# Performance work log

Measured on AMD Instinct MI355X. Metric: run time of the kernel, lower is better.

Reference implementation:

```python
import jax, jax.numpy as jnp
import numpy as np

N_ATOMS = 262144
BATCH = 4096
HIDDEN = 256
HEADS = 4
SCALE = (HIDDEN // HEADS) ** -0.5
LN_EPS = 1e-5
SM_EPS = 1e-16


def setup_inputs() -> dict:
    key = jax.random.key(0)
    ks = jax.random.split(key, 10)
    s = HIDDEN ** -0.5
    return {
        "drug_atoms": jax.random.normal(ks[0], (N_ATOMS, HIDDEN), jnp.float32),
        "protein_ctx": jax.random.normal(ks[1], (BATCH, HIDDEN), jnp.float32),
        "batch_index": jnp.sort(jax.random.randint(ks[2], (N_ATOMS,), 0, BATCH)),
        "Wq": jax.random.normal(ks[3], (HIDDEN, HIDDEN), jnp.float32) * s,
        "bq": jnp.zeros((HIDDEN,), jnp.float32),
        "Wk": jax.random.normal(ks[4], (HIDDEN, HIDDEN), jnp.float32) * s,
        "bk": jnp.zeros((HIDDEN,), jnp.float32),
        "Wv": jax.random.normal(ks[5], (HIDDEN, HIDDEN), jnp.float32) * s,
        "bv": jnp.zeros((HIDDEN,), jnp.float32),
        "ln_gamma": jnp.ones((HIDDEN,), jnp.float32),
        "ln_beta": jnp.zeros((HIDDEN,), jnp.float32),
    }


def _segment_softmax(logits, seg, num_segments):
    # logits: [N, 1]; segment-wise stable softmax (torch_geometric.utils.softmax)
    m = jax.ops.segment_max(logits, seg, num_segments=num_segments)  # [B, 1]
    e = jnp.exp(logits - m[seg])
    s = jax.ops.segment_sum(e, seg, num_segments=num_segments)  # [B, 1]
    return e / (s[seg] + SM_EPS)


def _layer_norm(x, gamma, beta):
    mu = jnp.mean(x, axis=-1, keepdims=True)
    var = jnp.mean(jnp.square(x - mu), axis=-1, keepdims=True)
    return (x - mu) * jax.lax.rsqrt(var + LN_EPS) * gamma + beta


def reference(drug_atoms, protein_ctx, batch_index, Wq, bq, Wk, bk, Wv, bv, ln_gamma, ln_beta):
    protein_expanded = protein_ctx[batch_index]  # [N, H] gather
    Q = protein_expanded @ Wq + bq
    K = drug_atoms @ Wk + bk
    V = drug_atoms @ Wv + bv
    dots = jnp.sum(Q * K, axis=-1, keepdims=True) * SCALE  # [N, 1]
    attn = _segment_softmax(dots, batch_index, BATCH)  # [N, 1]
    out = attn * V + drug_atoms  # weighted V + residual
    return _layer_norm(out, ln_gamma, ln_beta), attn
```

## Files before the change

### kernel.cpp

```cpp
#include <hip/hip_runtime.h>
#include <hip/hip_bf16.h>

#define N_ATOMS 262144
#define BATCH   4096
#define HID     256

typedef __attribute__((ext_vector_type(8))) short short8;
typedef __attribute__((ext_vector_type(4))) float f32x4;
typedef unsigned short u16;
typedef unsigned int   u32;

__device__ __forceinline__ float bf2f(u16 h){
    u32 x = ((u32)h) << 16;
    return __builtin_bit_cast(float, x);
}
__device__ __forceinline__ u16 f2bf(float f){
    u32 x = __builtin_bit_cast(u32, f);
    u32 r = (x + 0x7FFFu + ((x >> 16) & 1u)) >> 16;
    return (u16)r;
}
__device__ __forceinline__ int probe_isf32(const u32* p){
    return ((p[0] & 0xFFFFu) == 0u) ? 1 : 0;
}
__device__ __forceinline__ float cvt_any(const void* p, size_t i, int isf32){
    return isf32 ? ((const float*)p)[i] : bf2f(((const u16*)p)[i]);
}

__global__ void prep_kernel(const void* Wq, const void* Wk, const void* Wv,
                            const void* bq, const void* bk, const void* bv,
                            const void* gamma, const void* beta,
                            float* __restrict__ WqTF, float* __restrict__ WkF,
                            u16* __restrict__ WvT,
                            u32* __restrict__ menc, float* __restrict__ sbuf,
                            float* __restrict__ bqf, float* __restrict__ bkf,
                            float* __restrict__ bvf, float* __restrict__ gamf,
                            float* __restrict__ betf){
    const int isf32 = probe_isf32((const u32*)gamma);
    int blk = blockIdx.x, t = threadIdx.x;
    if (blk < 256){
        WqTF[blk*HID + t] = cvt_any(Wq, (size_t)t*HID + blk, isf32);
    } else if (blk < 512){
        size_t i = (size_t)(blk - 256)*256 + t;
        WkF[i] = cvt_any(Wk, i, isf32);
    } else if (blk < 768){
        int j = blk - 512;
        WvT[j*HID + t] = f2bf(cvt_any(Wv, (size_t)t*HID + j, isf32));
    } else if (blk < 784){
        int i = (blk - 768)*256 + t;
        menc[i] = 0u; sbuf[i] = 0.f;
    } else {
        bqf[t]  = cvt_any(bq, t, isf32);
        bkf[t]  = cvt_any(bk, t, isf32);
        bvf[t]  = cvt_any(bv, t, isf32);
        gamf[t] = cvt_any(gamma, t, isf32);
        betf[t] = cvt_any(beta, t, isf32);
    }
}

template<int AMODE, int BIAS>
__global__ void small_gemm(const void* Araw, const float* __restrict__ BtF,
                           const float* __restrict__ biasF,
                           float* __restrict__ outF, const u32* __restrict__ probe){
    __shared__ float As[8*HID];
    const int t  = threadIdx.x;
    const int rb = blockIdx.x * 8;
    const int isf32 = AMODE ? 1 : probe_isf32(probe);
    #pragma unroll
    for (int i = 0; i < 8; ++i)
        As[i*HID + t] = cvt_any(Araw, (size_t)(rb + i)*HID + t, isf32);
    __syncthreads();
    float acc[8] = {0.f,0.f,0.f,0.f,0.f,0.f,0.f,0.f};
    for (int j = 0; j < HID; j += 4){
        float4 w = *(const float4*)(BtF + (size_t)t*HID + j);
        #pragma unroll
        for (int r = 0; r < 8; ++r){
            float4 a = *(const float4*)(As + r*HID + j);
            acc[r] += a.x*w.x + a.y*w.y + a.z*w.z + a.w*w.w;
        }
    }
    float b = BIAS ? biasF[t] : 0.f;
    #pragma unroll
    for (int r = 0; r < 8; ++r)
        outF[(size_t)(rb + r)*HID + t] = acc[r] + b;
}

__global__ void ck_kernel(const float* __restrict__ Qf, const float* __restrict__ bkf,
                          float* __restrict__ cvec){
    int row  = blockIdx.x*4 + (threadIdx.x >> 6);
    int lane = threadIdx.x & 63;
    float4 q = *(const float4*)(Qf + (size_t)row*HID + lane*4);
    float p = q.x*bkf[lane*4] + q.y*bkf[lane*4+1] + q.z*bkf[lane*4+2] + q.w*bkf[lane*4+3];
    #pragma unroll
    for (int off=1; off<64; off<<=1) p += __shfl_xor(p, off, 64);
    if (lane == 0) cvec[row] = p;
}

__global__ void dots_kernel(const void* xraw, const int* __restrict__ bidx,
                            const float* __restrict__ uF, const float* __restrict__ cvec,
                            float* __restrict__ dots, u32* __restrict__ menc,
                            const u32* __restrict__ probe){
    const int isf32 = probe_isf32(probe);
    int row  = blockIdx.x*4 + (threadIdx.x >> 6);
    int lane = threadIdx.x & 63;
    int b = bidx[row];
    float4 uv = *(const float4*)(uF + (size_t)b*HID + lane*4);
    float p;
    if (isf32){
        float4 xv = *(const float4*)((const float*)xraw + (size_t)row*HID + lane*4);
        p = xv.x*uv.x + xv.y*uv.y + xv.z*uv.z + xv.w*uv.w;
    } else {
        ushort4 xv = *(const ushort4*)((const u16*)xraw + (size_t)row*HID + lane*4);
        p = bf2f(xv.x)*uv.x + bf2f(xv.y)*uv.y + bf2f(xv.z)*uv.z + bf2f(xv.w)*uv.w;
    }
    #pragma unroll
    for (int off=1; off<64; off<<=1) p += __shfl_xor(p, off, 64);
    if (lane == 0){
        float d = (p + cvec[b]) * 0.125f;
        if (!(fabsf(d) < 1e30f)) d = 0.f;
        dots[row] = d;
        u32 bits = __builtin_bit_cast(u32, d);
        u32 key = (bits & 0x80000000u) ? ~bits : (bits | 0x80000000u);
        atomicMax(&menc[b], key);
    }
}

__global__ void expsum_kernel(const int* __restrict__ bidx, const u32* __restrict__ menc,
                              float* __restrict__ dots, float* __restrict__ sbuf){
    int n    = blockIdx.x*256 + threadIdx.x;
    int lane = threadIdx.x & 63;
    int b = bidx[n];
    u32 key = menc[b];
    u32 bits = (key & 0x80000000u) ? (key & 0x7FFFFFFFu) : ~key;
    float m = __builtin_bit_cast(float, bits);
    float ev = __expf(dots[n] - m);
    dots[n] = ev;
    int b0  = __shfl(b, 0, 64);
    int b63 = __shfl(b, 63, 64);
    if (b0 == b63){
        float t = ev;
        #pragma unroll
        for (int off=1; off<64; off<<=1) t += __shfl_xor(t, off, 64);
        if (lane == 0) atomicAdd(&sbuf[b], t);
    } else {
        atomicAdd(&sbuf[b], ev);
    }
}

__launch_bounds__(256, 4)
__global__ void main_fused(const void* xraw, const u16* __restrict__ WvT,
                           const float* __restrict__ ebuf, const float* __restrict__ sbuf,
                           const int* __restrict__ bidx,
                           const float* __restrict__ bvf, const float* __restrict__ gamf,
                           const float* __restrict__ betf,
                           void* outraw, const u32* __restrict__ probe)
{
    __shared__ u16 Abuf[64*HID];
    __shared__ float attn_lds[64];
    __shared__ float bv_lds[HID];
    __shared__ float rowsum[64];
    __shared__ float rowsq[64];

    const int tid  = threadIdx.x;
    const int lane = tid & 63;
    const int wave = tid >> 6;
    const int quad = lane >> 4;
    const int l15  = lane & 15;
    const int rowBase = blockIdx.x * 64;
    const int isf32 = probe_isf32(probe);

    if (isf32){
        const float* Af = (const float*)xraw;
        #pragma unroll
        for (int iss = 0; iss < 8; ++iss){
            int g = iss*256 + tid; int r = g>>5, c = g&31;
            const float* p = Af + (size_t)(rowBase + r)*HID + c*8;
            float4 f0 = *(const float4*)p;
            float4 f1 = *(const float4*)(p + 4);
            short8 s;
            s[0]=(short)f2bf(f0.x); s[1]=(short)f2bf(f0.y);
            s[2]=(short)f2bf(f0.z); s[3]=(short)f2bf(f0.w);
            s[4]=(short)f2bf(f1.x); s[5]=(short)f2bf(f1.y);
            s[6]=(short)f2bf(f1.z); s[7]=(short)f2bf(f1.w);
            int cp = c ^ (r & 7);
            *(short8*)(Abuf + r*256 + cp*8) = s;
        }
    } else {
        const u16* Ab = (const u16*)xraw;
        short8 areg[8];
        #pragma unroll
        for (int iss = 0; iss < 8; ++iss){
            int g = iss*256 + tid; int r = g>>5, c = g&31;
            areg[iss] = *(const short8*)(Ab + (size_t)(rowBase + r)*HID + c*8);
        }
        #pragma unroll
        for (int iss = 0; iss < 8; ++iss){
            int g = iss*256 + tid; int r = g>>5, c = g&31;
            int cp = c ^ (r & 7);
            *(short8*)(Abuf + r*256 + cp*8) = areg[iss];
        }
    }

    if (tid < 64){
        int rowG = rowBase + tid;
        int b = bidx[rowG];
        float at = ebuf[rowG] / (sbuf[b] + 1e-16f);
        if (!(fabsf(at) < 1e30f)) at = 0.f;
        attn_lds[tid] = at;
        if (isf32) (((float*)outraw) + (size_t)N_ATOMS*HID)[rowG] = at;
        else       (((u16*)outraw)  + (size_t)N_ATOMS*HID)[rowG] = f2bf(at);
        rowsum[tid] = 0.f;
        rowsq[tid]  = 0.f;
    }
    bv_lds[tid] = bvf[tid];

    float gam[4], bet[4];
    #pragma unroll
    for (int ct = 0; ct < 4; ++ct){
        int col = wave*64 + ct*16 + l15;
        gam[ct] = gamf[col];
        bet[ct] = betf[col];
    }

    f32x4 acc[4][4];
    #pragma unroll
    for (int rt=0; rt<4; ++rt)
      #pragma unroll
      for (int ct=0; ct<4; ++ct)
        acc[rt][ct] = (f32x4){0.f,0.f,0.f,0.f};

    __syncthreads();

    for (int ki = 0; ki < 8; ++ki){
        short8 bfr[4];
        #pragma unroll
        for (int ct=0; ct<4; ++ct){
            int n = wave*64 + ct*16 + l15;
            bfr[ct] = *(const short8*)(WvT + (size_t)n*HID + ki*32 + quad*8);
        }
        short8 af[4];
        #pragma unroll
        for (int rt=0; rt<4; ++rt){
            int r  = rt*16 + l15;
            int cc = ki*4 + quad;
            int cp = cc ^ (r & 7);
            af[rt] = *(const short8*)(Abuf + r*256 + cp*8);
        }
        #pragma unroll
        for (int rt=0; rt<4; ++rt)
          #pragma unroll
          for (int ct=0; ct<4; ++ct)
            acc[rt][ct] = __builtin_amdgcn_mfma_f32_16x16x32_bf16(
                              af[rt], bfr[ct], acc[rt][ct], 0, 0, 0);
    }

    #pragma unroll
    for (int rt=0; rt<4; ++rt)
      #pragma unroll
      for (int ct=0; ct<4; ++ct)
        #pragma unroll
        for (int i=0; i<4; ++i){
            int row = rt*16 + quad*4 + i;
            int col = wave*64 + ct*16 + l15;
            int cc = col >> 3;
            int cp = cc ^ (row & 7);
            float xv = bf2f(Abuf[row*256 + cp*8 + (col & 7)]);
            acc[rt][ct][i] = attn_lds[row] * (acc[rt][ct][i] + bv_lds[col]) + xv;
        }
    #pragma unroll
    for (int rt=0; rt<4; ++rt)
      #pragma unroll
      for (int i=0; i<4; ++i){
          float s1 = 0.f, s2 = 0.f;
          #pragma unroll
          for (int ct=0; ct<4; ++ct){ float v = acc[rt][ct][i]; s1 += v; s2 += v*v; }
          #pragma unroll
          for (int off=1; off<16; off<<=1){
              s1 += __shfl_xor(s1, off, 64);
              s2 += __shfl_xor(s2, off, 64);
          }
          if (l15 == 0){
              int row = rt*16 + quad*4 + i;
              atomicAdd(&rowsum[row], s1);
              atomicAdd(&rowsq[row],  s2);
          }
      }
    __syncthreads();
    #pragma unroll
    for (int rt=0; rt<4; ++rt)
      #pragma unroll
      for (int i=0; i<4; ++i){
          int row = rt*16 + quad*4 + i;
          float mu  = rowsum[row] * (1.f/256.f);
          float var = fmaxf(rowsq[row] * (1.f/256.f) - mu*mu, 0.f);
          float rstd = rsqrtf(var + 1e-5f);
          #pragma unroll
          for (int ct=0; ct<4; ++ct){
              int col = wave*64 + ct*16 + l15;
              float v = (acc[rt][ct][i] - mu) * rstd * gam[ct] + bet[ct];
              size_t idx = (size_t)(rowBase+row)*HID + col;
              if (isf32) ((float*)outraw)[idx] = v;
              else       ((u16*)outraw)[idx]  = f2bf(v);
          }
      }
}

extern "C" void kernel_launch(void* const* d_in, const int* in_sizes, int n_in,
                              void* d_out, int out_size, void* d_ws, size_t ws_size,
                              hipStream_t stream) {
    const void* x    = d_in[0];
    const void* P    = d_in[1];
    const int*  bidx = (const int*)d_in[2];
    const void* Wq   = d_in[3];
    const void* bq   = d_in[4];
    const void* Wk   = d_in[5];
    const void* bk   = d_in[6];
    const void* Wv   = d_in[7];
    const void* bv   = d_in[8];
    const void* gam  = d_in[9];
    const void* bet  = d_in[10];
    const u32* probe = (const u32*)gam;

    char* ws = (char*)d_ws;
    float* WqTF = (float*)(ws);
    float* WkF  = (float*)(ws + 262144);
    u16*   WvT  = (u16*)  (ws + 524288);
    float* Qf   = (float*)(ws + 655360);
    float* uF   = (float*)(ws + 4849664);
    float* cvec = (float*)(ws + 9043968);
    u32*   menc = (u32*)  (ws + 9060352);
    float* sbuf = (float*)(ws + 9076736);
    float* dots = (float*)(ws + 9093120);
    float* bqf  = (float*)(ws + 10141696);
    float* bkf  = (float*)(ws + 10142720);
    float* bvf  = (float*)(ws + 10143744);
    float* gamf = (float*)(ws + 10144768);
    float* betf = (float*)(ws + 10145792);

    prep_kernel<<<785, 256, 0, stream>>>(Wq, Wk, Wv, bq, bk, bv, gam, bet,
                                         WqTF, WkF, WvT, menc, sbuf,
                                         bqf, bkf, bvf, gamf, betf);
    small_gemm<0,1><<<BATCH/8, 256, 0, stream>>>(P, WqTF, bqf, Qf, probe);
    small_gemm<1,0><<<BATCH/8, 256, 0, stream>>>(Qf, WkF, nullptr, uF, probe);
    ck_kernel<<<BATCH/4, 256, 0, stream>>>(Qf, bkf, cvec);
    dots_kernel<<<N_ATOMS/4, 256, 0, stream>>>(x, bidx, uF, cvec, dots, menc, probe);
    expsum_kernel<<<N_ATOMS/256, 256, 0, stream>>>(bidx, menc, dots, sbuf);
    main_fused<<<N_ATOMS/64, 256, 0, stream>>>(x, WvT, dots, sbuf, bidx,
                                               bvf, gamf, betf, d_out, probe);
}
```

Baseline: 848.5 us.

## Pre-swizzle Wv into MFMA fragment order and coalesce small GEMM weight reads

Wv is now stored in the order the MFMA B-fragments are consumed, so each wave reads one contiguous 1 KB chunk per fragment rather than strided 16-byte pieces from 16 rows. The small GEMMs now read weights in k-major layout, so threads read adjacent columns in a coalesced way instead of each thread reading float4s from its own row. Prep transposes are adjusted to match. This aims to cut global and L2 transaction overhead in the main fused kernel and the small GEMMs.

```diff
diff --git a/kernel.cpp b/kernel.cpp
--- a/kernel.cpp
+++ b/kernel.cpp
@@ -29,8 +29,8 @@
 __global__ void prep_kernel(const void* Wq, const void* Wk, const void* Wv,
                             const void* bq, const void* bk, const void* bv,
                             const void* gamma, const void* beta,
-                            float* __restrict__ WqTF, float* __restrict__ WkF,
-                            u16* __restrict__ WvT,
+                            float* __restrict__ WqF, float* __restrict__ WkTF,
+                            u16* __restrict__ Wfrag,
                             u32* __restrict__ menc, float* __restrict__ sbuf,
                             float* __restrict__ bqf, float* __restrict__ bkf,
                             float* __restrict__ bvf, float* __restrict__ gamf,
@@ -38,13 +38,18 @@
     const int isf32 = probe_isf32((const u32*)gamma);
     int blk = blockIdx.x, t = threadIdx.x;
     if (blk < 256){
-        WqTF[blk*HID + t] = cvt_any(Wq, (size_t)t*HID + blk, isf32);
+        size_t i = (size_t)blk*HID + t;
+        WqF[i] = cvt_any(Wq, i, isf32);
     } else if (blk < 512){
-        size_t i = (size_t)(blk - 256)*256 + t;
-        WkF[i] = cvt_any(Wk, i, isf32);
+        int k = blk - 256;
+        WkTF[(size_t)k*HID + t] = cvt_any(Wk, (size_t)t*HID + k, isf32);
     } else if (blk < 768){
-        int j = blk - 512;
-        WvT[j*HID + t] = f2bf(cvt_any(Wv, (size_t)t*HID + j, isf32));
+        int n = blk - 512;
+        int k = t;
+        int ntile = n >> 4, l15 = n & 15;
+        int ki = k >> 5, quad = (k >> 3) & 3, e = k & 7;
+        int off = ((ntile*8 + ki)*4 + quad)*128 + l15*8 + e;
+        Wfrag[off] = f2bf(cvt_any(Wv, (size_t)k*HID + n, isf32));
     } else if (blk < 784){
         int i = (blk - 768)*256 + t;
         menc[i] = 0u; sbuf[i] = 0.f;
@@ -58,7 +63,7 @@
 }
 
 template<int AMODE, int BIAS>
-__global__ void small_gemm(const void* Araw, const float* __restrict__ BtF,
+__global__ void small_gemm(const void* Araw, const float* __restrict__ BknF,
                            const float* __restrict__ biasF,
                            float* __restrict__ outF, const u32* __restrict__ probe){
     __shared__ float As[8*HID];
@@ -71,11 +76,14 @@
     __syncthreads();
     float acc[8] = {0.f,0.f,0.f,0.f,0.f,0.f,0.f,0.f};
     for (int j = 0; j < HID; j += 4){
-        float4 w = *(const float4*)(BtF + (size_t)t*HID + j);
+        float w0 = BknF[(size_t)(j+0)*HID + t];
+        float w1 = BknF[(size_t)(j+1)*HID + t];
+        float w2 = BknF[(size_t)(j+2)*HID + t];
+        float w3 = BknF[(size_t)(j+3)*HID + t];
         #pragma unroll
         for (int r = 0; r < 8; ++r){
             float4 a = *(const float4*)(As + r*HID + j);
-            acc[r] += a.x*w.x + a.y*w.y + a.z*w.z + a.w*w.w;
+            acc[r] += a.x*w0 + a.y*w1 + a.z*w2 + a.w*w3;
         }
     }
     float b = BIAS ? biasF[t] : 0.f;
@@ -147,7 +155,7 @@
 }
 
 __launch_bounds__(256, 4)
-__global__ void main_fused(const void* xraw, const u16* __restrict__ WvT,
+__global__ void main_fused(const void* xraw, const u16* __restrict__ Wfrag,
                            const float* __restrict__ ebuf, const float* __restrict__ sbuf,
                            const int* __restrict__ bidx,
                            const float* __restrict__ bvf, const float* __restrict__ gamf,
@@ -234,8 +242,8 @@
         short8 bfr[4];
         #pragma unroll
         for (int ct=0; ct<4; ++ct){
-            int n = wave*64 + ct*16 + l15;
-            bfr[ct] = *(const short8*)(WvT + (size_t)n*HID + ki*32 + quad*8);
+            int ntile = wave*4 + ct;
+            bfr[ct] = *(const short8*)(Wfrag + (size_t)((ntile*8 + ki)*512) + lane*8);
         }
         short8 af[4];
         #pragma unroll
@@ -321,9 +329,9 @@
     const u32* probe = (const u32*)gam;
 
     char* ws = (char*)d_ws;
-    float* WqTF = (float*)(ws);
-    float* WkF  = (float*)(ws + 262144);
-    u16*   WvT  = (u16*)  (ws + 524288);
+    float* WqF  = (float*)(ws);
+    float* WkTF = (float*)(ws + 262144);
+    u16*   Wfrag= (u16*)  (ws + 524288);
     float* Qf   = (float*)(ws + 655360);
     float* uF   = (float*)(ws + 4849664);
     float* cvec = (float*)(ws + 9043968);
@@ -337,13 +345,13 @@
     float* betf = (float*)(ws + 10145792);
 
     prep_kernel<<<785, 256, 0, stream>>>(Wq, Wk, Wv, bq, bk, bv, gam, bet,
-                                         WqTF, WkF, WvT, menc, sbuf,
+                                         WqF, WkTF, Wfrag, menc, sbuf,
                                          bqf, bkf, bvf, gamf, betf);
-    small_gemm<0,1><<<BATCH/8, 256, 0, stream>>>(P, WqTF, bqf, Qf, probe);
-    small_gemm<1,0><<<BATCH/8, 256, 0, stream>>>(Qf, WkF, nullptr, uF, probe);
+    small_gemm<0,1><<<BATCH/8, 256, 0, stream>>>(P, WqF, bqf, Qf, probe);
+    small_gemm<1,0><<<BATCH/8, 256, 0, stream>>>(Qf, WkTF, nullptr, uF, probe);
     ck_kernel<<<BATCH/4, 256, 0, stream>>>(Qf, bkf, cvec);
     dots_kernel<<<N_ATOMS/4, 256, 0, stream>>>(x, bidx, uF, cvec, dots, menc, probe);
     expsum_kernel<<<N_ATOMS/256, 256, 0, stream>>>(bidx, menc, dots, sbuf);
-    main_fused<<<N_ATOMS/64, 256, 0, stream>>>(x, WvT, dots, sbuf, bidx,
+    main_fused<<<N_ATOMS/64, 256, 0, stream>>>(x, Wfrag, dots, sbuf, bidx,
                                                bvf, gamf, betf, d_out, probe);
 }
```

Measured after the change: 820.1 us. 1.03x faster.
